# Kernel optimization log

Hardware: AMD Instinct MI355X
Metric: run time of the kernel (lower is better)

The kernel has to match this reference:

```python
import jax, jax.numpy as jnp
import numpy as np

K, S, B, D = 6, 257, 64, 1024   # blocks, seq, batch, d_model
H, DR = 16, 256                  # heads, pruned dim (d_model/reduction)
HD = DR // H                     # head_dim = 16
T = 0.1
EPS = 1e-5


def _ln(x, w, b):
    mu = jnp.mean(x, axis=-1, keepdims=True)
    var = jnp.var(x, axis=-1, keepdims=True)
    return (x - mu) * jax.lax.rsqrt(var + EPS) * w + b


def _quick_gelu(x):
    return x * jax.nn.sigmoid(1.702 * x)


def _block(x, ipw, ipb, opw, opb, l1w, l1b, l2w, l2b, fw, fb, cw, cb):
    # x: (S, B, D)
    h = _ln(x, l1w, l1b)
    qkv = jnp.einsum('sbe,fe->sbf', h, ipw) + ipb          # (S, B, 3*DR)
    q, k, v = jnp.split(qkv, 3, axis=-1)                    # each (S, B, DR)
    # (S, B*H, HD) -> (B*H, S, HD); row-major reshape matches torch .view
    q = q.reshape(S, B * H, HD).swapaxes(0, 1) / jnp.sqrt(jnp.asarray(HD, x.dtype))
    k = k.reshape(S, B * H, HD).swapaxes(0, 1)
    v = v.reshape(S, B * H, HD).swapaxes(0, 1)
    attn = jax.nn.softmax(jnp.einsum('bte,bse->bts', q, k), axis=-1)  # (B*H, S, S)
    o = jnp.einsum('bts,bse->bte', attn, v)                 # (B*H, S, HD)
    o = o.swapaxes(0, 1).reshape(S, B, DR)
    o = jnp.einsum('sbe,fe->sbf', o, opw) + opb             # (S, B, D)
    x = x + o
    h2 = _ln(x, l2w, l2b)
    m = _quick_gelu(jnp.einsum('sbe,fe->sbf', h2, fw) + fb)
    m = jnp.einsum('sbe,fe->sbf', m, cw) + cb
    return x + m


def setup_inputs() -> dict:
    key = jax.random.key(0)
    ks = jax.random.split(key, 10)
    p = 0.02
    return {
        'hook_inputs': jax.random.normal(ks[0], (K, S, B, D), jnp.float32),
        'alpha': jax.random.normal(ks[1], (K,), jnp.float32),
        'in_proj_w': jax.random.normal(ks[2], (K, 3 * DR, D), jnp.float32) * p,
        'in_proj_b': jnp.zeros((K, 3 * DR), jnp.float32),
        'out_proj_w': jax.random.normal(ks[3], (K, D, DR), jnp.float32) * p,
        'out_proj_b': jnp.zeros((K, D), jnp.float32),
        'ln1_w': jnp.ones((K, D), jnp.float32),
        'ln1_b': jnp.zeros((K, D), jnp.float32),
        'ln2_w': jnp.ones((K, D), jnp.float32),
        'ln2_b': jnp.zeros((K, D), jnp.float32),
        'fc_w': jax.random.normal(ks[4], (K, D, D), jnp.float32) * p,
        'fc_b': jnp.zeros((K, D), jnp.float32),
        'cproj_w': jax.random.normal(ks[5], (K, D, D), jnp.float32) * p,
        'cproj_b': jnp.zeros((K, D), jnp.float32),
        'ln_post_w': jnp.ones((D,), jnp.float32),
        'ln_post_b': jnp.zeros((D,), jnp.float32),
        'proj': jax.random.normal(ks[6], (D, 768), jnp.float32) * p,
    }


def reference(hook_inputs, alpha, in_proj_w, in_proj_b, out_proj_w, out_proj_b,
              ln1_w, ln1_b, ln2_w, ln2_b, fc_w, fc_b, cproj_w, cproj_b,
              ln_post_w, ln_post_b, proj):
    Wm = jax.nn.sigmoid(alpha / T)
    x = None
    for i in range(K):  # small fixed number of structurally distinct blocks
        res = hook_inputs[i]
        if i == 0:
            x = res
        else:
            x = Wm[i] * res + (1.0 - Wm[i]) * x
        x = _block(x, in_proj_w[i], in_proj_b[i], out_proj_w[i], out_proj_b[i],
                   ln1_w[i], ln1_b[i], ln2_w[i], ln2_b[i],
                   fc_w[i], fc_b[i], cproj_w[i], cproj_b[i])
    x = x.transpose(1, 0, 2)                 # (B, S, D)
    x = _ln(x, ln_post_w, ln_post_b)
    x = jnp.einsum('bsd,dp->bsp', x, proj)   # (B, S, 768)
    return x
```

## Files before the change

kernel.cpp:

```cpp
#include <hip/hip_runtime.h>
#include <hip/hip_bf16.h>
#include <cstdint>
#include <cstddef>

#define KBLK 6
#define SL 257
#define BA 64
#define DM 1024
#define NHEAD 16
#define DRED 256
#define HDM 16
#define MR (SL * BA)
#define MP 16512
#define LNEPS 1e-5f

typedef __hip_bfloat16 bf16;
typedef __attribute__((ext_vector_type(8))) short short8;
typedef __attribute__((ext_vector_type(4))) short short4_t;
typedef __attribute__((ext_vector_type(4))) float f32x4;

__device__ __forceinline__ void gld_lds16(const void* g, void* l) {
  __builtin_amdgcn_global_load_lds(
      (const __attribute__((address_space(1))) unsigned int*)g,
      (__attribute__((address_space(3))) unsigned int*)l, 16, 0, 0);
}

__device__ __forceinline__ float bf2f(short s) {
  bf16 t = *reinterpret_cast<bf16*>(&s);
  return __bfloat162float(t);
}
__device__ __forceinline__ short f2bf(float f) {
  bf16 t = __float2bfloat16(f);
  return *reinterpret_cast<short*>(&t);
}

__global__ __launch_bounds__(256) void cast_all_kernel(
    const float* __restrict__ ipw, const float* __restrict__ opw,
    const float* __restrict__ fcw, const float* __restrict__ cpw,
    const float* __restrict__ proj,
    bf16* __restrict__ wq, bf16* __restrict__ wo, bf16* __restrict__ wfc,
    bf16* __restrict__ wcp, bf16* __restrict__ wpj) {
  const int blk = blockIdx.x;
  const int tid = threadIdx.x;
  const float* src;
  bf16* dst;
  int base;
  bool tr = false;
  if (blk < 2304)      { src = ipw; dst = wq;  base = blk * 2048; }
  else if (blk < 3072) { src = opw; dst = wo;  base = (blk - 2304) * 2048; }
  else if (blk < 6144) { src = fcw; dst = wfc; base = (blk - 3072) * 2048; }
  else if (blk < 9216) { src = cpw; dst = wcp; base = (blk - 6144) * 2048; }
  else                 { src = proj; dst = wpj; base = (blk - 9216) * 2048; tr = true; }
  const int idx = base + tid * 8;
  short8 o;
  if (!tr) {
    float4 a = *(const float4*)(src + idx);
    float4 b = *(const float4*)(src + idx + 4);
    o[0] = f2bf(a.x); o[1] = f2bf(a.y); o[2] = f2bf(a.z); o[3] = f2bf(a.w);
    o[4] = f2bf(b.x); o[5] = f2bf(b.y); o[6] = f2bf(b.z); o[7] = f2bf(b.w);
  } else {
    int n = idx >> 10, k = idx & 1023;
#pragma unroll
    for (int e = 0; e < 8; ++e) o[e] = f2bf(src[(size_t)(k + e) * 768 + n]);
  }
  *(short8*)(dst + idx) = o;
}

template <int MODE>
__global__ __launch_bounds__(256) void ln_kernel(
    const float* __restrict__ hook,
    bf16* __restrict__ x, bf16* __restrict__ hout,
    const float* __restrict__ w, const float* __restrict__ bb) {
  const int row = blockIdx.x;
  const int tid = threadIdx.x;
  const size_t base = (size_t)row * DM + tid * 4;
  float vals[4];
  if (MODE == 0) {
    float4 v = *(const float4*)(hook + base);
    vals[0] = v.x; vals[1] = v.y; vals[2] = v.z; vals[3] = v.w;
    short4_t pk;
#pragma unroll
    for (int j = 0; j < 4; ++j) pk[j] = f2bf(vals[j]);
    *(short4_t*)&x[base] = pk;
  } else {
    short4_t xv = *(const short4_t*)&x[base];
#pragma unroll
    for (int j = 0; j < 4; ++j) vals[j] = bf2f(xv[j]);
  }
  float s1 = vals[0] + vals[1] + vals[2] + vals[3];
  float s2 = vals[0] * vals[0] + vals[1] * vals[1] + vals[2] * vals[2] + vals[3] * vals[3];
#pragma unroll
  for (int o = 32; o >= 1; o >>= 1) {
    s1 += __shfl_down(s1, o);
    s2 += __shfl_down(s2, o);
  }
  __shared__ float red[8];
  if ((tid & 63) == 0) {
    red[tid >> 6] = s1;
    red[4 + (tid >> 6)] = s2;
  }
  __syncthreads();
  s1 = red[0] + red[1] + red[2] + red[3];
  s2 = red[4] + red[5] + red[6] + red[7];
  const float mu = s1 * (1.f / DM);
  const float rs = rsqrtf(s2 * (1.f / DM) - mu * mu + LNEPS);
  size_t orow = row;
  if (MODE == 3) {
    int s = row >> 6, b2 = row & 63;
    orow = (size_t)b2 * SL + s;
  }
  const int c = tid * 4;
  short4_t pk;
#pragma unroll
  for (int j = 0; j < 4; ++j)
    pk[j] = f2bf((vals[j] - mu) * rs * w[c + j] + bb[c + j]);
  *(short4_t*)((char*)hout + (orow * DM + c) * 2) = pk;
}

__global__ __launch_bounds__(256) void attn_mfma_kernel(const bf16* __restrict__ qkv,
                                                        bf16* __restrict__ obuf) {
  __shared__ __align__(16) short ql[272][24];
  __shared__ __align__(16) short kl[272][24];
  __shared__ __align__(16) short vt[16][296];
  __shared__ __align__(16) short pl[4][16][40];
  const int bh = blockIdx.x;
  const int b = bh >> 4, h = bh & 15;
  const int tid = threadIdx.x;
  const int wave = tid >> 6, lane = tid & 63;
  const int g = lane >> 4, qi = lane & 15;

  const short8 zero8 = {0, 0, 0, 0, 0, 0, 0, 0};
  const f32x4 fzero = {0.f, 0.f, 0.f, 0.f};

  for (int task = tid; task < 1632; task += 256) {
    int a, rem;
    if (task < 544) { a = 0; rem = task; }
    else if (task < 1088) { a = 1; rem = task - 544; }
    else { a = 2; rem = task - 1088; }
    int row = rem >> 1, half = rem & 1;
    short8 v = zero8;
    if (row < SL)
      v = *(const short8*)((const short*)qkv + (size_t)(row * BA + b) * 768 + a * 256 + h * 16 + half * 8);
    if (a == 0) *(short8*)&ql[row][half * 8] = v;
    else if (a == 1) *(short8*)&kl[row][half * 8] = v;
    else {
#pragma unroll
      for (int j = 0; j < 8; ++j) vt[half * 8 + j][row] = v[j];
    }
  }
  for (int i = tid; i < 16 * 24; i += 256) vt[i / 24][272 + (i % 24)] = 0;
  __syncthreads();

  for (int t = wave; t < 17; t += 4) {
    short8 bq = zero8;
    if (g < 2) bq = *(const short8*)&ql[t * 16 + qi][g * 8];

    f32x4 st[18];
#pragma unroll
    for (int t2 = 0; t2 < 17; ++t2) {
      short8 ak = zero8;
      if (g < 2) ak = *(const short8*)&kl[t2 * 16 + qi][g * 8];
      st[t2] = __builtin_amdgcn_mfma_f32_16x16x32_bf16(ak, bq, fzero, 0, 0, 0);
    }
    float mx = -1e30f;
#pragma unroll
    for (int t2 = 0; t2 < 17; ++t2) {
#pragma unroll
      for (int r = 0; r < 4; ++r) {
        int s = t2 * 16 + g * 4 + r;
        float v = (s <= 256) ? st[t2][r] * 0.25f : -1e30f;
        st[t2][r] = v;
        mx = fmaxf(mx, v);
      }
    }
    mx = fmaxf(mx, __shfl_xor(mx, 16));
    mx = fmaxf(mx, __shfl_xor(mx, 32));
    float ls = 0.f;
#pragma unroll
    for (int t2 = 0; t2 < 17; ++t2) {
#pragma unroll
      for (int r = 0; r < 4; ++r) {
        float p = __expf(st[t2][r] - mx);
        st[t2][r] = p;
        ls += p;
      }
    }
    ls += __shfl_xor(ls, 16);
    ls += __shfl_xor(ls, 32);
    const float inv = 1.f / ls;
#pragma unroll
    for (int t2 = 0; t2 < 17; ++t2)
#pragma unroll
      for (int r = 0; r < 4; ++r) st[t2][r] *= inv;
    st[17] = fzero;

    f32x4 acc = fzero;
#pragma unroll
    for (int tt = 0; tt < 9; ++tt) {
#pragma unroll
      for (int hh = 0; hh < 2; ++hh) {
        int t2 = tt * 2 + hh;
        short4_t pk;
#pragma unroll
        for (int r = 0; r < 4; ++r) pk[r] = f2bf(st[t2][r]);
        *(short4_t*)&pl[wave][qi][hh * 16 + g * 4] = pk;
      }
      short8 pa = *(const short8*)&pl[wave][qi][g * 8];
      short8 bv = *(const short8*)&vt[qi][tt * 32 + g * 8];
      acc = __builtin_amdgcn_mfma_f32_16x16x32_bf16(pa, bv, acc, 0, 0, 0);
    }
#pragma unroll
    for (int r = 0; r < 4; ++r) {
      int qr = t * 16 + g * 4 + r;
      if (qr < SL)
        obuf[(size_t)(qr * BA + b) * DRED + h * 16 + qi] = __float2bfloat16(acc[r]);
    }
  }
}

template <int EPI>
__global__ __launch_bounds__(256, 4) void gemm_kernel(
    const bf16* __restrict__ A, int lda,
    const bf16* __restrict__ Bw, int ldb,
    const float* __restrict__ bias,
    void* __restrict__ C, int ldc,
    int Kdim, int Mreal,
    const float* __restrict__ hook, const float* __restrict__ alphap, int kidx) {
  __shared__ char lds[32768];
  const int tid = threadIdx.x;
  const int wave = tid >> 6, lane = tid & 63;
  const int lrow = lane & 15, lk = lane >> 4;
  const int wr = wave >> 1, wc = wave & 1;

  const int gx = gridDim.x, gy = gridDim.y;
  const int nwg = gx * gy;
  const int orig = blockIdx.y * gx + blockIdx.x;
  const int q = nwg >> 3, r = nwg & 7;
  const int xcd = orig & 7, idx = orig >> 3;
  const int wgid = (xcd < r ? xcd * (q + 1) : r * (q + 1) + (xcd - r) * q) + idx;
  const int m0 = (wgid / gy) * 128;
  const int n0 = (wgid % gy) * 128;

  f32x4 acc[4][4];
  const f32x4 zero = {0.f, 0.f, 0.f, 0.f};
#pragma unroll
  for (int i = 0; i < 4; ++i)
#pragma unroll
    for (int j = 0; j < 4; ++j) acc[i][j] = zero;

  const int nk = Kdim >> 6;

  for (int kt = 0; kt < nk; ++kt) {
    const int k0 = kt << 6;
#pragma unroll
    for (int j = 0; j < 4; ++j) {
      int c = wave * 256 + j * 64 + lane;
      int row = c >> 3, segp = c & 7;
      int seg = segp ^ (row & 7);
      const bf16* ga = A + (size_t)(m0 + row) * lda + k0 + seg * 8;
      gld_lds16(ga, &lds[(wave * 256 + j * 64) * 16]);
      const bf16* gb = Bw + (size_t)(n0 + row) * ldb + k0 + seg * 8;
      gld_lds16(gb, &lds[16384 + (wave * 256 + j * 64) * 16]);
    }
    __syncthreads();
    const char* aL = &lds[0];
    const char* bL = aL + 16384;
#pragma unroll
    for (int kh = 0; kh < 2; ++kh) {
      short8 af[4], bfr[4];
#pragma unroll
      for (int i = 0; i < 4; ++i) {
        int rr = wr * 64 + i * 16 + lrow;
        int seg = kh * 4 + lk;
        af[i] = *(const short8*)(aL + rr * 128 + ((seg ^ (rr & 7)) << 4));
      }
#pragma unroll
      for (int j = 0; j < 4; ++j) {
        int rr = wc * 64 + j * 16 + lrow;
        int seg = kh * 4 + lk;
        bfr[j] = *(const short8*)(bL + rr * 128 + ((seg ^ (rr & 7)) << 4));
      }
#pragma unroll
      for (int i = 0; i < 4; ++i)
#pragma unroll
        for (int j = 0; j < 4; ++j)
          acc[i][j] = __builtin_amdgcn_mfma_f32_16x16x32_bf16(bfr[j], af[i], acc[i][j], 0, 0, 0);
    }
    __syncthreads();
  }

  float wmg = 0.f, omg = 0.f;
  if (EPI == 4) {
    wmg = 1.f / (1.f + __expf(-alphap[kidx] * 10.f));
    omg = 1.f - wmg;
  }
#pragma unroll
  for (int i = 0; i < 4; ++i) {
    const int row = m0 + wr * 64 + i * 16 + lrow;
    if (row >= Mreal) continue;
#pragma unroll
    for (int j = 0; j < 4; ++j) {
      const int col = n0 + wc * 64 + j * 16 + lk * 4;
      const size_t off = (size_t)row * ldc + col;
      float bv[4] = {0.f, 0.f, 0.f, 0.f};
      if (bias) {
        float4 b4 = *(const float4*)&bias[col];
        bv[0] = b4.x; bv[1] = b4.y; bv[2] = b4.z; bv[3] = b4.w;
      }
      float v[4];
#pragma unroll
      for (int rr = 0; rr < 4; ++rr) v[rr] = acc[i][j][rr] + bv[rr];
      if (EPI == 0) {
        float4 o4 = {v[0], v[1], v[2], v[3]};
        *(float4*)((float*)C + off) = o4;
      } else if (EPI == 2) {
        short4_t pk;
#pragma unroll
        for (int rr = 0; rr < 4; ++rr)
          pk[rr] = f2bf(v[rr] / (1.f + __expf(-1.702f * v[rr])));
        *(short4_t*)((bf16*)C + off) = pk;
      } else if (EPI == 3) {
        short4_t pk;
#pragma unroll
        for (int rr = 0; rr < 4; ++rr) pk[rr] = f2bf(v[rr]);
        *(short4_t*)((bf16*)C + off) = pk;
      } else if (EPI == 1) {
        short4_t xv = *(const short4_t*)((const bf16*)C + off);
        short4_t pk;
#pragma unroll
        for (int rr = 0; rr < 4; ++rr) pk[rr] = f2bf(bf2f(xv[rr]) + v[rr]);
        *(short4_t*)((bf16*)C + off) = pk;
      } else {
        short4_t xv = *(const short4_t*)((const bf16*)C + off);
        float4 h4 = *(const float4*)&hook[off];
        float hk[4] = {h4.x, h4.y, h4.z, h4.w};
        short4_t pk;
#pragma unroll
        for (int rr = 0; rr < 4; ++rr)
          pk[rr] = f2bf(wmg * hk[rr] + omg * (bf2f(xv[rr]) + v[rr]));
        *(short4_t*)((bf16*)C + off) = pk;
      }
    }
  }
}

extern "C" void kernel_launch(void* const* d_in, const int* in_sizes, int n_in,
                              void* d_out, int out_size, void* d_ws, size_t ws_size,
                              hipStream_t stream) {
  const float* hook = (const float*)d_in[0];
  const float* alpha = (const float*)d_in[1];
  const float* ipw = (const float*)d_in[2];
  const float* ipb = (const float*)d_in[3];
  const float* opw = (const float*)d_in[4];
  const float* opb = (const float*)d_in[5];
  const float* l1w = (const float*)d_in[6];
  const float* l1b = (const float*)d_in[7];
  const float* l2w = (const float*)d_in[8];
  const float* l2b = (const float*)d_in[9];
  const float* fcw = (const float*)d_in[10];
  const float* fcb = (const float*)d_in[11];
  const float* cpw = (const float*)d_in[12];
  const float* cpb = (const float*)d_in[13];
  const float* lpw = (const float*)d_in[14];
  const float* lpb = (const float*)d_in[15];
  const float* proj = (const float*)d_in[16];

  char* ws = (char*)d_ws;
  size_t off = 0;
  bf16* x = (bf16*)(ws + off); off += (size_t)MP * DM * 2;
  bf16* hbuf = (bf16*)(ws + off); off += (size_t)MP * DM * 2;
  bf16* qkv = (bf16*)(ws + off);
  bf16* mbuf = (bf16*)qkv;
  off += (size_t)MP * 1024 * 2;
  bf16* obuf = (bf16*)(ws + off); off += (size_t)MP * DRED * 2;
  bf16* wq = (bf16*)(ws + off); off += (size_t)KBLK * 768 * DM * 2;
  bf16* wo = (bf16*)(ws + off); off += (size_t)KBLK * DM * DRED * 2;
  bf16* wfc = (bf16*)(ws + off); off += (size_t)KBLK * DM * DM * 2;
  bf16* wcp = (bf16*)(ws + off); off += (size_t)KBLK * DM * DM * 2;
  bf16* wpj = (bf16*)(ws + off); off += (size_t)768 * DM * 2;

  cast_all_kernel<<<9600, 256, 0, stream>>>(ipw, opw, fcw, cpw, proj,
                                            wq, wo, wfc, wcp, wpj);

  const dim3 gq(MP / 128, 768 / 128);
  const dim3 gm(MP / 128, DM / 128);

  for (int i = 0; i < KBLK; ++i) {
    if (i == 0)
      ln_kernel<0><<<MR, 256, 0, stream>>>(hook, x, hbuf, l1w, l1b);
    else
      ln_kernel<2><<<MR, 256, 0, stream>>>(nullptr, x, hbuf, l1w + i * DM, l1b + i * DM);
    gemm_kernel<3><<<gq, 256, 0, stream>>>(hbuf, DM, wq + (size_t)i * 768 * DM, DM,
                                           ipb + i * 768, qkv, 768, DM, MR,
                                           nullptr, nullptr, 0);
    attn_mfma_kernel<<<BA * NHEAD, 256, 0, stream>>>(qkv, obuf);
    gemm_kernel<1><<<gm, 256, 0, stream>>>(obuf, DRED, wo + (size_t)i * DM * DRED, DRED,
                                           opb + i * DM, x, DM, DRED, MR,
                                           nullptr, nullptr, 0);
    ln_kernel<2><<<MR, 256, 0, stream>>>(nullptr, x, hbuf, l2w + i * DM, l2b + i * DM);
    gemm_kernel<2><<<gm, 256, 0, stream>>>(hbuf, DM, wfc + (size_t)i * DM * DM, DM,
                                           fcb + i * DM, mbuf, DM, DM, MR,
                                           nullptr, nullptr, 0);
    if (i + 1 < KBLK)
      gemm_kernel<4><<<gm, 256, 0, stream>>>(mbuf, DM, wcp + (size_t)i * DM * DM, DM,
                                             cpb + i * DM, x, DM, DM, MR,
                                             hook + (size_t)(i + 1) * MR * DM, alpha, i + 1);
    else
      gemm_kernel<1><<<gm, 256, 0, stream>>>(mbuf, DM, wcp + (size_t)i * DM * DM, DM,
                                             cpb + i * DM, x, DM, DM, MR,
                                             nullptr, nullptr, 0);
  }
  ln_kernel<3><<<MR, 256, 0, stream>>>(nullptr, x, hbuf, lpw, lpb);
  gemm_kernel<0><<<gq, 256, 0, stream>>>(hbuf, DM, wpj, DM, nullptr,
                                         (float*)d_out, 768, DM, MR,
                                         nullptr, nullptr, 0);
}
```

Measured before the change: 1.797 ms.

## Fuse all per-block kernels into one persistent cooperative megakernel with grid syncs

```diff
diff --git a/kernel.cpp b/kernel.cpp
--- a/kernel.cpp
+++ b/kernel.cpp
@@ -1,7 +1,10 @@
 #include <hip/hip_runtime.h>
 #include <hip/hip_bf16.h>
+#include <hip/hip_cooperative_groups.h>
 #include <cstdint>
 #include <cstddef>
+
+namespace cg = cooperative_groups;
 
 #define KBLK 6
 #define SL 257
@@ -66,282 +69,326 @@
   *(short8*)(dst + idx) = o;
 }
 
-template <int MODE>
-__global__ __launch_bounds__(256) void ln_kernel(
-    const float* __restrict__ hook,
-    bf16* __restrict__ x, bf16* __restrict__ hout,
-    const float* __restrict__ w, const float* __restrict__ bb) {
-  const int row = blockIdx.x;
+union __align__(16) MegaLds {
+  char gemm[32768];
+  struct {
+    short kl[272][24];
+    short vt[16][296];
+    short pl[4][16][40];
+  } at;
+  float red[8];
+};
+
+__device__ __forceinline__ void ph_ln(int mode, int nwg, int wg,
+    const float* __restrict__ hk, bf16* __restrict__ x, bf16* __restrict__ hout,
+    const float* __restrict__ w, const float* __restrict__ bb, float* red) {
   const int tid = threadIdx.x;
-  const size_t base = (size_t)row * DM + tid * 4;
-  float vals[4];
-  if (MODE == 0) {
-    float4 v = *(const float4*)(hook + base);
-    vals[0] = v.x; vals[1] = v.y; vals[2] = v.z; vals[3] = v.w;
+  for (int row = wg; row < MR; row += nwg) {
+    const size_t base = (size_t)row * DM + tid * 4;
+    float vals[4];
+    if (mode == 0) {
+      float4 v = *(const float4*)(hk + base);
+      vals[0] = v.x; vals[1] = v.y; vals[2] = v.z; vals[3] = v.w;
+      short4_t pk;
+#pragma unroll
+      for (int j = 0; j < 4; ++j) pk[j] = f2bf(vals[j]);
+      *(short4_t*)&x[base] = pk;
+    } else {
+      short4_t xv = *(const short4_t*)&x[base];
+#pragma unroll
+      for (int j = 0; j < 4; ++j) vals[j] = bf2f(xv[j]);
+    }
+    float s1 = vals[0] + vals[1] + vals[2] + vals[3];
+    float s2 = vals[0] * vals[0] + vals[1] * vals[1] + vals[2] * vals[2] + vals[3] * vals[3];
+#pragma unroll
+    for (int o = 32; o >= 1; o >>= 1) {
+      s1 += __shfl_down(s1, o);
+      s2 += __shfl_down(s2, o);
+    }
+    if ((tid & 63) == 0) {
+      red[tid >> 6] = s1;
+      red[4 + (tid >> 6)] = s2;
+    }
+    __syncthreads();
+    s1 = red[0] + red[1] + red[2] + red[3];
+    s2 = red[4] + red[5] + red[6] + red[7];
+    const float mu = s1 * (1.f / DM);
+    const float rs = rsqrtf(s2 * (1.f / DM) - mu * mu + LNEPS);
+    size_t orow = row;
+    if (mode == 3) {
+      int s = row >> 6, b2 = row & 63;
+      orow = (size_t)b2 * SL + s;
+    }
+    const int c = tid * 4;
     short4_t pk;
 #pragma unroll
-    for (int j = 0; j < 4; ++j) pk[j] = f2bf(vals[j]);
-    *(short4_t*)&x[base] = pk;
-  } else {
-    short4_t xv = *(const short4_t*)&x[base];
-#pragma unroll
-    for (int j = 0; j < 4; ++j) vals[j] = bf2f(xv[j]);
-  }
-  float s1 = vals[0] + vals[1] + vals[2] + vals[3];
-  float s2 = vals[0] * vals[0] + vals[1] * vals[1] + vals[2] * vals[2] + vals[3] * vals[3];
-#pragma unroll
-  for (int o = 32; o >= 1; o >>= 1) {
-    s1 += __shfl_down(s1, o);
-    s2 += __shfl_down(s2, o);
-  }
-  __shared__ float red[8];
-  if ((tid & 63) == 0) {
-    red[tid >> 6] = s1;
-    red[4 + (tid >> 6)] = s2;
-  }
-  __syncthreads();
-  s1 = red[0] + red[1] + red[2] + red[3];
-  s2 = red[4] + red[5] + red[6] + red[7];
-  const float mu = s1 * (1.f / DM);
-  const float rs = rsqrtf(s2 * (1.f / DM) - mu * mu + LNEPS);
-  size_t orow = row;
-  if (MODE == 3) {
-    int s = row >> 6, b2 = row & 63;
-    orow = (size_t)b2 * SL + s;
-  }
-  const int c = tid * 4;
-  short4_t pk;
-#pragma unroll
-  for (int j = 0; j < 4; ++j)
-    pk[j] = f2bf((vals[j] - mu) * rs * w[c + j] + bb[c + j]);
-  *(short4_t*)((char*)hout + (orow * DM + c) * 2) = pk;
-}
-
-__global__ __launch_bounds__(256) void attn_mfma_kernel(const bf16* __restrict__ qkv,
-                                                        bf16* __restrict__ obuf) {
-  __shared__ __align__(16) short ql[272][24];
-  __shared__ __align__(16) short kl[272][24];
-  __shared__ __align__(16) short vt[16][296];
-  __shared__ __align__(16) short pl[4][16][40];
-  const int bh = blockIdx.x;
-  const int b = bh >> 4, h = bh & 15;
+    for (int j = 0; j < 4; ++j)
+      pk[j] = f2bf((vals[j] - mu) * rs * w[c + j] + bb[c + j]);
+    *(short4_t*)((char*)hout + (orow * DM + c) * 2) = pk;
+    __syncthreads();
+  }
+}
+
+__device__ __forceinline__ void ph_attn(int nwg, int wg, MegaLds* L,
+                                        const bf16* __restrict__ qkv,
+                                        bf16* __restrict__ obuf) {
   const int tid = threadIdx.x;
   const int wave = tid >> 6, lane = tid & 63;
   const int g = lane >> 4, qi = lane & 15;
-
   const short8 zero8 = {0, 0, 0, 0, 0, 0, 0, 0};
   const f32x4 fzero = {0.f, 0.f, 0.f, 0.f};
 
-  for (int task = tid; task < 1632; task += 256) {
-    int a, rem;
-    if (task < 544) { a = 0; rem = task; }
-    else if (task < 1088) { a = 1; rem = task - 544; }
-    else { a = 2; rem = task - 1088; }
-    int row = rem >> 1, half = rem & 1;
-    short8 v = zero8;
-    if (row < SL)
-      v = *(const short8*)((const short*)qkv + (size_t)(row * BA + b) * 768 + a * 256 + h * 16 + half * 8);
-    if (a == 0) *(short8*)&ql[row][half * 8] = v;
-    else if (a == 1) *(short8*)&kl[row][half * 8] = v;
-    else {
-#pragma unroll
-      for (int j = 0; j < 8; ++j) vt[half * 8 + j][row] = v[j];
-    }
-  }
-  for (int i = tid; i < 16 * 24; i += 256) vt[i / 24][272 + (i % 24)] = 0;
-  __syncthreads();
-
-  for (int t = wave; t < 17; t += 4) {
-    short8 bq = zero8;
-    if (g < 2) bq = *(const short8*)&ql[t * 16 + qi][g * 8];
-
-    f32x4 st[18];
-#pragma unroll
-    for (int t2 = 0; t2 < 17; ++t2) {
-      short8 ak = zero8;
-      if (g < 2) ak = *(const short8*)&kl[t2 * 16 + qi][g * 8];
-      st[t2] = __builtin_amdgcn_mfma_f32_16x16x32_bf16(ak, bq, fzero, 0, 0, 0);
-    }
-    float mx = -1e30f;
-#pragma unroll
-    for (int t2 = 0; t2 < 17; ++t2) {
+  for (int bh = wg; bh < BA * NHEAD; bh += nwg) {
+    const int b = bh >> 4, h = bh & 15;
+    for (int task = tid; task < 1088; task += 256) {
+      int a = (task < 544) ? 1 : 2;
+      int rem = (task < 544) ? task : task - 544;
+      int row = rem >> 1, half = rem & 1;
+      short8 v = zero8;
+      if (row < SL)
+        v = *(const short8*)((const short*)qkv + (size_t)(row * BA + b) * 768 + a * 256 + h * 16 + half * 8);
+      if (a == 1) *(short8*)&L->at.kl[row][half * 8] = v;
+      else {
+#pragma unroll
+        for (int j = 0; j < 8; ++j) L->at.vt[half * 8 + j][row] = v[j];
+      }
+    }
+    for (int i = tid; i < 16 * 24; i += 256) L->at.vt[i / 24][272 + (i % 24)] = 0;
+    __syncthreads();
+
+    for (int t = wave; t < 17; t += 4) {
+      const int qrow = t * 16 + qi;
+      short8 bq = zero8;
+      if (g < 2 && qrow < SL)
+        bq = *(const short8*)((const short*)qkv + (size_t)(qrow * BA + b) * 768 + h * 16 + g * 8);
+
+      f32x4 st[18];
+#pragma unroll
+      for (int t2 = 0; t2 < 17; ++t2) {
+        short8 ak = zero8;
+        if (g < 2) ak = *(const short8*)&L->at.kl[t2 * 16 + qi][g * 8];
+        st[t2] = __builtin_amdgcn_mfma_f32_16x16x32_bf16(ak, bq, fzero, 0, 0, 0);
+      }
+      float mx = -1e30f;
+#pragma unroll
+      for (int t2 = 0; t2 < 17; ++t2) {
+#pragma unroll
+        for (int r = 0; r < 4; ++r) {
+          int s = t2 * 16 + g * 4 + r;
+          float v = (s <= 256) ? st[t2][r] * 0.25f : -1e30f;
+          st[t2][r] = v;
+          mx = fmaxf(mx, v);
+        }
+      }
+      mx = fmaxf(mx, __shfl_xor(mx, 16));
+      mx = fmaxf(mx, __shfl_xor(mx, 32));
+      float ls = 0.f;
+#pragma unroll
+      for (int t2 = 0; t2 < 17; ++t2) {
+#pragma unroll
+        for (int r = 0; r < 4; ++r) {
+          float p = __expf(st[t2][r] - mx);
+          st[t2][r] = p;
+          ls += p;
+        }
+      }
+      ls += __shfl_xor(ls, 16);
+      ls += __shfl_xor(ls, 32);
+      const float inv = 1.f / ls;
+#pragma unroll
+      for (int t2 = 0; t2 < 17; ++t2)
+#pragma unroll
+        for (int r = 0; r < 4; ++r) st[t2][r] *= inv;
+      st[17] = fzero;
+
+      f32x4 acc = fzero;
+#pragma unroll
+      for (int tt = 0; tt < 9; ++tt) {
+#pragma unroll
+        for (int hh = 0; hh < 2; ++hh) {
+          int t2 = tt * 2 + hh;
+          short4_t pk;
+#pragma unroll
+          for (int r = 0; r < 4; ++r) pk[r] = f2bf(st[t2][r]);
+          *(short4_t*)&L->at.pl[wave][qi][hh * 16 + g * 4] = pk;
+        }
+        short8 pa = *(const short8*)&L->at.pl[wave][qi][g * 8];
+        short8 bv = *(const short8*)&L->at.vt[qi][tt * 32 + g * 8];
+        acc = __builtin_amdgcn_mfma_f32_16x16x32_bf16(pa, bv, acc, 0, 0, 0);
+      }
 #pragma unroll
       for (int r = 0; r < 4; ++r) {
-        int s = t2 * 16 + g * 4 + r;
-        float v = (s <= 256) ? st[t2][r] * 0.25f : -1e30f;
-        st[t2][r] = v;
-        mx = fmaxf(mx, v);
-      }
-    }
-    mx = fmaxf(mx, __shfl_xor(mx, 16));
-    mx = fmaxf(mx, __shfl_xor(mx, 32));
-    float ls = 0.f;
-#pragma unroll
-    for (int t2 = 0; t2 < 17; ++t2) {
-#pragma unroll
-      for (int r = 0; r < 4; ++r) {
-        float p = __expf(st[t2][r] - mx);
-        st[t2][r] = p;
-        ls += p;
-      }
-    }
-    ls += __shfl_xor(ls, 16);
-    ls += __shfl_xor(ls, 32);
-    const float inv = 1.f / ls;
-#pragma unroll
-    for (int t2 = 0; t2 < 17; ++t2)
-#pragma unroll
-      for (int r = 0; r < 4; ++r) st[t2][r] *= inv;
-    st[17] = fzero;
-
-    f32x4 acc = fzero;
-#pragma unroll
-    for (int tt = 0; tt < 9; ++tt) {
-#pragma unroll
-      for (int hh = 0; hh < 2; ++hh) {
-        int t2 = tt * 2 + hh;
-        short4_t pk;
-#pragma unroll
-        for (int r = 0; r < 4; ++r) pk[r] = f2bf(st[t2][r]);
-        *(short4_t*)&pl[wave][qi][hh * 16 + g * 4] = pk;
-      }
-      short8 pa = *(const short8*)&pl[wave][qi][g * 8];
-      short8 bv = *(const short8*)&vt[qi][tt * 32 + g * 8];
-      acc = __builtin_amdgcn_mfma_f32_16x16x32_bf16(pa, bv, acc, 0, 0, 0);
-    }
-#pragma unroll
-    for (int r = 0; r < 4; ++r) {
-      int qr = t * 16 + g * 4 + r;
-      if (qr < SL)
-        obuf[(size_t)(qr * BA + b) * DRED + h * 16 + qi] = __float2bfloat16(acc[r]);
-    }
+        int qr = t * 16 + g * 4 + r;
+        if (qr < SL)
+          obuf[(size_t)(qr * BA + b) * DRED + h * 16 + qi] = __float2bfloat16(acc[r]);
+      }
+    }
+    __syncthreads();
   }
 }
 
 template <int EPI>
-__global__ __launch_bounds__(256, 4) void gemm_kernel(
+__device__ __forceinline__ void ph_gemm(int nwg, int wg, char* lds,
     const bf16* __restrict__ A, int lda,
     const bf16* __restrict__ Bw, int ldb,
     const float* __restrict__ bias,
     void* __restrict__ C, int ldc,
-    int Kdim, int Mreal,
+    int Kdim, int nT, int ntiles,
     const float* __restrict__ hook, const float* __restrict__ alphap, int kidx) {
-  __shared__ char lds[32768];
   const int tid = threadIdx.x;
   const int wave = tid >> 6, lane = tid & 63;
   const int lrow = lane & 15, lk = lane >> 4;
   const int wr = wave >> 1, wc = wave & 1;
-
-  const int gx = gridDim.x, gy = gridDim.y;
-  const int nwg = gx * gy;
-  const int orig = blockIdx.y * gx + blockIdx.x;
-  const int q = nwg >> 3, r = nwg & 7;
-  const int xcd = orig & 7, idx = orig >> 3;
-  const int wgid = (xcd < r ? xcd * (q + 1) : r * (q + 1) + (xcd - r) * q) + idx;
-  const int m0 = (wgid / gy) * 128;
-  const int n0 = (wgid % gy) * 128;
-
-  f32x4 acc[4][4];
-  const f32x4 zero = {0.f, 0.f, 0.f, 0.f};
-#pragma unroll
-  for (int i = 0; i < 4; ++i)
-#pragma unroll
-    for (int j = 0; j < 4; ++j) acc[i][j] = zero;
-
+  const int q = ntiles >> 3, r = ntiles & 7;
   const int nk = Kdim >> 6;
-
-  for (int kt = 0; kt < nk; ++kt) {
-    const int k0 = kt << 6;
-#pragma unroll
-    for (int j = 0; j < 4; ++j) {
-      int c = wave * 256 + j * 64 + lane;
-      int row = c >> 3, segp = c & 7;
-      int seg = segp ^ (row & 7);
-      const bf16* ga = A + (size_t)(m0 + row) * lda + k0 + seg * 8;
-      gld_lds16(ga, &lds[(wave * 256 + j * 64) * 16]);
-      const bf16* gb = Bw + (size_t)(n0 + row) * ldb + k0 + seg * 8;
-      gld_lds16(gb, &lds[16384 + (wave * 256 + j * 64) * 16]);
-    }
-    __syncthreads();
-    const char* aL = &lds[0];
-    const char* bL = aL + 16384;
-#pragma unroll
-    for (int kh = 0; kh < 2; ++kh) {
-      short8 af[4], bfr[4];
-#pragma unroll
-      for (int i = 0; i < 4; ++i) {
-        int rr = wr * 64 + i * 16 + lrow;
-        int seg = kh * 4 + lk;
-        af[i] = *(const short8*)(aL + rr * 128 + ((seg ^ (rr & 7)) << 4));
-      }
-#pragma unroll
-      for (int j = 0; j < 4; ++j) {
-        int rr = wc * 64 + j * 16 + lrow;
-        int seg = kh * 4 + lk;
-        bfr[j] = *(const short8*)(bL + rr * 128 + ((seg ^ (rr & 7)) << 4));
-      }
-#pragma unroll
-      for (int i = 0; i < 4; ++i)
-#pragma unroll
-        for (int j = 0; j < 4; ++j)
-          acc[i][j] = __builtin_amdgcn_mfma_f32_16x16x32_bf16(bfr[j], af[i], acc[i][j], 0, 0, 0);
-    }
-    __syncthreads();
-  }
 
   float wmg = 0.f, omg = 0.f;
   if (EPI == 4) {
     wmg = 1.f / (1.f + __expf(-alphap[kidx] * 10.f));
     omg = 1.f - wmg;
   }
-#pragma unroll
-  for (int i = 0; i < 4; ++i) {
-    const int row = m0 + wr * 64 + i * 16 + lrow;
-    if (row >= Mreal) continue;
-#pragma unroll
-    for (int j = 0; j < 4; ++j) {
-      const int col = n0 + wc * 64 + j * 16 + lk * 4;
-      const size_t off = (size_t)row * ldc + col;
-      float bv[4] = {0.f, 0.f, 0.f, 0.f};
-      if (bias) {
-        float4 b4 = *(const float4*)&bias[col];
-        bv[0] = b4.x; bv[1] = b4.y; bv[2] = b4.z; bv[3] = b4.w;
-      }
-      float v[4];
-#pragma unroll
-      for (int rr = 0; rr < 4; ++rr) v[rr] = acc[i][j][rr] + bv[rr];
-      if (EPI == 0) {
-        float4 o4 = {v[0], v[1], v[2], v[3]};
-        *(float4*)((float*)C + off) = o4;
-      } else if (EPI == 2) {
-        short4_t pk;
-#pragma unroll
-        for (int rr = 0; rr < 4; ++rr)
-          pk[rr] = f2bf(v[rr] / (1.f + __expf(-1.702f * v[rr])));
-        *(short4_t*)((bf16*)C + off) = pk;
-      } else if (EPI == 3) {
-        short4_t pk;
-#pragma unroll
-        for (int rr = 0; rr < 4; ++rr) pk[rr] = f2bf(v[rr]);
-        *(short4_t*)((bf16*)C + off) = pk;
-      } else if (EPI == 1) {
-        short4_t xv = *(const short4_t*)((const bf16*)C + off);
-        short4_t pk;
-#pragma unroll
-        for (int rr = 0; rr < 4; ++rr) pk[rr] = f2bf(bf2f(xv[rr]) + v[rr]);
-        *(short4_t*)((bf16*)C + off) = pk;
-      } else {
-        short4_t xv = *(const short4_t*)((const bf16*)C + off);
-        float4 h4 = *(const float4*)&hook[off];
-        float hk[4] = {h4.x, h4.y, h4.z, h4.w};
-        short4_t pk;
-#pragma unroll
-        for (int rr = 0; rr < 4; ++rr)
-          pk[rr] = f2bf(wmg * hk[rr] + omg * (bf2f(xv[rr]) + v[rr]));
-        *(short4_t*)((bf16*)C + off) = pk;
-      }
-    }
-  }
+
+  for (int t0 = wg; t0 < ntiles; t0 += nwg) {
+    const int xcd = t0 & 7, idx = t0 >> 3;
+    const int wgid = (xcd < r ? xcd * (q + 1) : r * (q + 1) + (xcd - r) * q) + idx;
+    const int m0 = (wgid / nT) * 128;
+    const int n0 = (wgid % nT) * 128;
+
+    f32x4 acc[4][4];
+    const f32x4 zero = {0.f, 0.f, 0.f, 0.f};
+#pragma unroll
+    for (int i = 0; i < 4; ++i)
+#pragma unroll
+      for (int j = 0; j < 4; ++j) acc[i][j] = zero;
+
+    for (int kt = 0; kt < nk; ++kt) {
+      const int k0 = kt << 6;
+#pragma unroll
+      for (int j = 0; j < 4; ++j) {
+        int c = wave * 256 + j * 64 + lane;
+        int row = c >> 3, segp = c & 7;
+        int seg = segp ^ (row & 7);
+        gld_lds16(A + (size_t)(m0 + row) * lda + k0 + seg * 8, &lds[c * 16]);
+        gld_lds16(Bw + (size_t)(n0 + row) * ldb + k0 + seg * 8, &lds[16384 + c * 16]);
+      }
+      __syncthreads();
+#pragma unroll
+      for (int kh = 0; kh < 2; ++kh) {
+        short8 af[4], bfr[4];
+#pragma unroll
+        for (int i = 0; i < 4; ++i) {
+          int rr = wr * 64 + i * 16 + lrow;
+          int seg = kh * 4 + lk;
+          af[i] = *(const short8*)(lds + rr * 128 + ((seg ^ (rr & 7)) << 4));
+        }
+#pragma unroll
+        for (int j = 0; j < 4; ++j) {
+          int rr = wc * 64 + j * 16 + lrow;
+          int seg = kh * 4 + lk;
+          bfr[j] = *(const short8*)(lds + 16384 + rr * 128 + ((seg ^ (rr & 7)) << 4));
+        }
+#pragma unroll
+        for (int i = 0; i < 4; ++i)
+#pragma unroll
+          for (int j = 0; j < 4; ++j)
+            acc[i][j] = __builtin_amdgcn_mfma_f32_16x16x32_bf16(bfr[j], af[i], acc[i][j], 0, 0, 0);
+      }
+      __syncthreads();
+    }
+
+#pragma unroll
+    for (int i = 0; i < 4; ++i) {
+      const int row = m0 + wr * 64 + i * 16 + lrow;
+      if (row >= MR) continue;
+#pragma unroll
+      for (int j = 0; j < 4; ++j) {
+        const int col = n0 + wc * 64 + j * 16 + lk * 4;
+        const size_t off = (size_t)row * ldc + col;
+        float bv[4] = {0.f, 0.f, 0.f, 0.f};
+        if (bias) {
+          float4 b4 = *(const float4*)&bias[col];
+          bv[0] = b4.x; bv[1] = b4.y; bv[2] = b4.z; bv[3] = b4.w;
+        }
+        float v[4];
+#pragma unroll
+        for (int rr = 0; rr < 4; ++rr) v[rr] = acc[i][j][rr] + bv[rr];
+        if (EPI == 0) {
+          float4 o4 = {v[0], v[1], v[2], v[3]};
+          *(float4*)((float*)C + off) = o4;
+        } else if (EPI == 2) {
+          short4_t pk;
+#pragma unroll
+          for (int rr = 0; rr < 4; ++rr)
+            pk[rr] = f2bf(v[rr] / (1.f + __expf(-1.702f * v[rr])));
+          *(short4_t*)((bf16*)C + off) = pk;
+        } else if (EPI == 3) {
+          short4_t pk;
+#pragma unroll
+          for (int rr = 0; rr < 4; ++rr) pk[rr] = f2bf(v[rr]);
+          *(short4_t*)((bf16*)C + off) = pk;
+        } else if (EPI == 1) {
+          short4_t xv = *(const short4_t*)((const bf16*)C + off);
+          short4_t pk;
+#pragma unroll
+          for (int rr = 0; rr < 4; ++rr) pk[rr] = f2bf(bf2f(xv[rr]) + v[rr]);
+          *(short4_t*)((bf16*)C + off) = pk;
+        } else {
+          short4_t xv = *(const short4_t*)((const bf16*)C + off);
+          float4 h4 = *(const float4*)&hook[off];
+          float hk[4] = {h4.x, h4.y, h4.z, h4.w};
+          short4_t pk;
+#pragma unroll
+          for (int rr = 0; rr < 4; ++rr)
+            pk[rr] = f2bf(wmg * hk[rr] + omg * (bf2f(xv[rr]) + v[rr]));
+          *(short4_t*)((bf16*)C + off) = pk;
+        }
+      }
+    }
+  }
+}
+
+__global__ __launch_bounds__(256, 4) void mega_kernel(
+    const float* hook, const float* alpha,
+    const float* ipb, const float* opb,
+    const float* l1w, const float* l1b, const float* l2w, const float* l2b,
+    const float* fcb, const float* cpb, const float* lpw, const float* lpb,
+    bf16* x, bf16* hbuf, bf16* qkv, bf16* obuf,
+    const bf16* wq, const bf16* wo, const bf16* wfc, const bf16* wcp, const bf16* wpj,
+    float* outp) {
+  cg::grid_group grid = cg::this_grid();
+  __shared__ MegaLds L;
+  const int wg = blockIdx.x, nwg = gridDim.x;
+  bf16* mbuf = qkv;
+
+  for (int i = 0; i < KBLK; ++i) {
+    ph_ln(i == 0 ? 0 : 2, nwg, wg, hook, x, hbuf, l1w + i * DM, l1b + i * DM, L.red);
+    grid.sync();
+    ph_gemm<3>(nwg, wg, L.gemm, hbuf, DM, wq + (size_t)i * 768 * DM, DM,
+               ipb + i * 768, qkv, 768, DM, 6, 774, nullptr, nullptr, 0);
+    grid.sync();
+    ph_attn(nwg, wg, &L, qkv, obuf);
+    grid.sync();
+    ph_gemm<1>(nwg, wg, L.gemm, obuf, DRED, wo + (size_t)i * DM * DRED, DRED,
+               opb + i * DM, x, DM, DRED, 8, 1032, nullptr, nullptr, 0);
+    grid.sync();
+    ph_ln(2, nwg, wg, nullptr, x, hbuf, l2w + i * DM, l2b + i * DM, L.red);
+    grid.sync();
+    ph_gemm<2>(nwg, wg, L.gemm, hbuf, DM, wfc + (size_t)i * DM * DM, DM,
+               fcb + i * DM, mbuf, DM, DM, 8, 1032, nullptr, nullptr, 0);
+    grid.sync();
+    if (i + 1 < KBLK)
+      ph_gemm<4>(nwg, wg, L.gemm, mbuf, DM, wcp + (size_t)i * DM * DM, DM,
+                 cpb + i * DM, x, DM, DM, 8, 1032,
+                 hook + (size_t)(i + 1) * MR * DM, alpha, i + 1);
+    else
+      ph_gemm<1>(nwg, wg, L.gemm, mbuf, DM, wcp + (size_t)i * DM * DM, DM,
+                 cpb + i * DM, x, DM, DM, 8, 1032, nullptr, nullptr, 0);
+    grid.sync();
+  }
+  ph_ln(3, nwg, wg, nullptr, x, hbuf, lpw, lpb, L.red);
+  grid.sync();
+  ph_gemm<0>(nwg, wg, L.gemm, hbuf, DM, wpj, DM, nullptr,
+             outp, 768, DM, 6, 774, nullptr, nullptr, 0);
 }
 
 extern "C" void kernel_launch(void* const* d_in, const int* in_sizes, int n_in,
@@ -369,9 +416,7 @@
   size_t off = 0;
   bf16* x = (bf16*)(ws + off); off += (size_t)MP * DM * 2;
   bf16* hbuf = (bf16*)(ws + off); off += (size_t)MP * DM * 2;
-  bf16* qkv = (bf16*)(ws + off);
-  bf16* mbuf = (bf16*)qkv;
-  off += (size_t)MP * 1024 * 2;
+  bf16* qkv = (bf16*)(ws + off); off += (size_t)MP * 1024 * 2;
   bf16* obuf = (bf16*)(ws + off); off += (size_t)MP * DRED * 2;
   bf16* wq = (bf16*)(ws + off); off += (size_t)KBLK * 768 * DM * 2;
   bf16* wo = (bf16*)(ws + off); off += (size_t)KBLK * DM * DRED * 2;
@@ -382,36 +427,20 @@
   cast_all_kernel<<<9600, 256, 0, stream>>>(ipw, opw, fcw, cpw, proj,
                                             wq, wo, wfc, wcp, wpj);
 
-  const dim3 gq(MP / 128, 768 / 128);
-  const dim3 gm(MP / 128, DM / 128);
-
-  for (int i = 0; i < KBLK; ++i) {
-    if (i == 0)
-      ln_kernel<0><<<MR, 256, 0, stream>>>(hook, x, hbuf, l1w, l1b);
-    else
-      ln_kernel<2><<<MR, 256, 0, stream>>>(nullptr, x, hbuf, l1w + i * DM, l1b + i * DM);
-    gemm_kernel<3><<<gq, 256, 0, stream>>>(hbuf, DM, wq + (size_t)i * 768 * DM, DM,
-                                           ipb + i * 768, qkv, 768, DM, MR,
-                                           nullptr, nullptr, 0);
-    attn_mfma_kernel<<<BA * NHEAD, 256, 0, stream>>>(qkv, obuf);
-    gemm_kernel<1><<<gm, 256, 0, stream>>>(obuf, DRED, wo + (size_t)i * DM * DRED, DRED,
-                                           opb + i * DM, x, DM, DRED, MR,
-                                           nullptr, nullptr, 0);
-    ln_kernel<2><<<MR, 256, 0, stream>>>(nullptr, x, hbuf, l2w + i * DM, l2b + i * DM);
-    gemm_kernel<2><<<gm, 256, 0, stream>>>(hbuf, DM, wfc + (size_t)i * DM * DM, DM,
-                                           fcb + i * DM, mbuf, DM, DM, MR,
-                                           nullptr, nullptr, 0);
-    if (i + 1 < KBLK)
-      gemm_kernel<4><<<gm, 256, 0, stream>>>(mbuf, DM, wcp + (size_t)i * DM * DM, DM,
-                                             cpb + i * DM, x, DM, DM, MR,
-                                             hook + (size_t)(i + 1) * MR * DM, alpha, i + 1);
-    else
-      gemm_kernel<1><<<gm, 256, 0, stream>>>(mbuf, DM, wcp + (size_t)i * DM * DM, DM,
-                                             cpb + i * DM, x, DM, DM, MR,
-                                             nullptr, nullptr, 0);
-  }
-  ln_kernel<3><<<MR, 256, 0, stream>>>(nullptr, x, hbuf, lpw, lpb);
-  gemm_kernel<0><<<gq, 256, 0, stream>>>(hbuf, DM, wpj, DM, nullptr,
-                                         (float*)d_out, 768, DM, MR,
-                                         nullptr, nullptr, 0);
-}
+  int occ = 0;
+  hipOccupancyMaxActiveBlocksPerMultiprocessor(&occ, mega_kernel, 256, 0);
+  int gw = occ * 256;
+  if (gw > 1024) gw = 1024;
+  if (gw < 256) gw = 256;
+  float* outp = (float*)d_out;
+
+  void* params[] = {
+      (void*)&hook, (void*)&alpha, (void*)&ipb, (void*)&opb,
+      (void*)&l1w, (void*)&l1b, (void*)&l2w, (void*)&l2b,
+      (void*)&fcb, (void*)&cpb, (void*)&lpw, (void*)&lpb,
+      (void*)&x, (void*)&hbuf, (void*)&qkv, (void*)&obuf,
+      (void*)&wq, (void*)&wo, (void*)&wfc, (void*)&wcp, (void*)&wpj,
+      (void*)&outp};
+  hipLaunchCooperativeKernel((void*)mega_kernel, dim3(gw), dim3(256),
+                             params, 0, stream);
+}
```

Result: slower. 5.144 ms (+186.3%).

## Fuse LayerNorm into residual GEMM epilogues via last-block-per-panel counters

Applied to the files above, without the earlier changes.

```diff
diff --git a/kernel.cpp b/kernel.cpp
--- a/kernel.cpp
+++ b/kernel.cpp
@@ -13,6 +13,8 @@
 #define MR (SL * BA)
 #define MP 16512
 #define LNEPS 1e-5f
+#define NPANEL 129
+#define NCNT (12 * NPANEL)
 
 typedef __hip_bfloat16 bf16;
 typedef __attribute__((ext_vector_type(8))) short short8;
@@ -39,9 +41,12 @@
     const float* __restrict__ fcw, const float* __restrict__ cpw,
     const float* __restrict__ proj,
     bf16* __restrict__ wq, bf16* __restrict__ wo, bf16* __restrict__ wfc,
-    bf16* __restrict__ wcp, bf16* __restrict__ wpj) {
+    bf16* __restrict__ wcp, bf16* __restrict__ wpj, int* __restrict__ cnt) {
   const int blk = blockIdx.x;
   const int tid = threadIdx.x;
+  if (blk == 0) {
+    for (int z = tid; z < NCNT; z += 256) cnt[z] = 0;
+  }
   const float* src;
   bf16* dst;
   int base;
@@ -66,8 +71,7 @@
   *(short8*)(dst + idx) = o;
 }
 
-template <int MODE>
-__global__ __launch_bounds__(256) void ln_kernel(
+__global__ __launch_bounds__(256) void ln0_kernel(
     const float* __restrict__ hook,
     bf16* __restrict__ x, bf16* __restrict__ hout,
     const float* __restrict__ w, const float* __restrict__ bb) {
@@ -75,18 +79,12 @@
   const int tid = threadIdx.x;
   const size_t base = (size_t)row * DM + tid * 4;
   float vals[4];
-  if (MODE == 0) {
-    float4 v = *(const float4*)(hook + base);
-    vals[0] = v.x; vals[1] = v.y; vals[2] = v.z; vals[3] = v.w;
-    short4_t pk;
-#pragma unroll
-    for (int j = 0; j < 4; ++j) pk[j] = f2bf(vals[j]);
-    *(short4_t*)&x[base] = pk;
-  } else {
-    short4_t xv = *(const short4_t*)&x[base];
-#pragma unroll
-    for (int j = 0; j < 4; ++j) vals[j] = bf2f(xv[j]);
-  }
+  float4 v = *(const float4*)(hook + base);
+  vals[0] = v.x; vals[1] = v.y; vals[2] = v.z; vals[3] = v.w;
+  short4_t pk0;
+#pragma unroll
+  for (int j = 0; j < 4; ++j) pk0[j] = f2bf(vals[j]);
+  *(short4_t*)&x[base] = pk0;
   float s1 = vals[0] + vals[1] + vals[2] + vals[3];
   float s2 = vals[0] * vals[0] + vals[1] * vals[1] + vals[2] * vals[2] + vals[3] * vals[3];
 #pragma unroll
@@ -104,17 +102,12 @@
   s2 = red[4] + red[5] + red[6] + red[7];
   const float mu = s1 * (1.f / DM);
   const float rs = rsqrtf(s2 * (1.f / DM) - mu * mu + LNEPS);
-  size_t orow = row;
-  if (MODE == 3) {
-    int s = row >> 6, b2 = row & 63;
-    orow = (size_t)b2 * SL + s;
-  }
   const int c = tid * 4;
   short4_t pk;
 #pragma unroll
   for (int j = 0; j < 4; ++j)
     pk[j] = f2bf((vals[j] - mu) * rs * w[c + j] + bb[c + j]);
-  *(short4_t*)((char*)hout + (orow * DM + c) * 2) = pk;
+  *(short4_t*)((char*)hout + ((size_t)row * DM + c) * 2) = pk;
 }
 
 __global__ __launch_bounds__(256) void attn_mfma_kernel(const bf16* __restrict__ qkv,
@@ -218,14 +211,16 @@
   }
 }
 
-template <int EPI>
+template <int EPI, int FLN>
 __global__ __launch_bounds__(256, 4) void gemm_kernel(
     const bf16* __restrict__ A, int lda,
     const bf16* __restrict__ Bw, int ldb,
     const float* __restrict__ bias,
     void* __restrict__ C, int ldc,
     int Kdim, int Mreal,
-    const float* __restrict__ hook, const float* __restrict__ alphap, int kidx) {
+    const float* __restrict__ hook, const float* __restrict__ alphap, int kidx,
+    const float* __restrict__ lnw, const float* __restrict__ lnb,
+    bf16* __restrict__ lnout, int* __restrict__ cnt) {
   __shared__ char lds[32768];
   const int tid = threadIdx.x;
   const int wave = tid >> 6, lane = tid & 63;
@@ -257,14 +252,10 @@
       int c = wave * 256 + j * 64 + lane;
       int row = c >> 3, segp = c & 7;
       int seg = segp ^ (row & 7);
-      const bf16* ga = A + (size_t)(m0 + row) * lda + k0 + seg * 8;
-      gld_lds16(ga, &lds[(wave * 256 + j * 64) * 16]);
-      const bf16* gb = Bw + (size_t)(n0 + row) * ldb + k0 + seg * 8;
-      gld_lds16(gb, &lds[16384 + (wave * 256 + j * 64) * 16]);
+      gld_lds16(A + (size_t)(m0 + row) * lda + k0 + seg * 8, &lds[c * 16]);
+      gld_lds16(Bw + (size_t)(n0 + row) * ldb + k0 + seg * 8, &lds[16384 + c * 16]);
     }
     __syncthreads();
-    const char* aL = &lds[0];
-    const char* bL = aL + 16384;
 #pragma unroll
     for (int kh = 0; kh < 2; ++kh) {
       short8 af[4], bfr[4];
@@ -272,13 +263,13 @@
       for (int i = 0; i < 4; ++i) {
         int rr = wr * 64 + i * 16 + lrow;
         int seg = kh * 4 + lk;
-        af[i] = *(const short8*)(aL + rr * 128 + ((seg ^ (rr & 7)) << 4));
+        af[i] = *(const short8*)(lds + rr * 128 + ((seg ^ (rr & 7)) << 4));
       }
 #pragma unroll
       for (int j = 0; j < 4; ++j) {
         int rr = wc * 64 + j * 16 + lrow;
         int seg = kh * 4 + lk;
-        bfr[j] = *(const short8*)(bL + rr * 128 + ((seg ^ (rr & 7)) << 4));
+        bfr[j] = *(const short8*)(lds + 16384 + rr * 128 + ((seg ^ (rr & 7)) << 4));
       }
 #pragma unroll
       for (int i = 0; i < 4; ++i)
@@ -339,6 +330,59 @@
         for (int rr = 0; rr < 4; ++rr)
           pk[rr] = f2bf(wmg * hk[rr] + omg * (bf2f(xv[rr]) + v[rr]));
         *(short4_t*)((bf16*)C + off) = pk;
+      }
+    }
+  }
+
+  if (FLN != 0) {
+    __shared__ int lastf;
+    __threadfence();
+    if (tid == 0)
+      lastf = (atomicAdd(&cnt[m0 >> 7], 1) == (int)gy - 1) ? 1 : 0;
+    __syncthreads();
+    if (lastf) {
+      __threadfence();
+      const bf16* xr = (const bf16*)C;
+      for (int r2 = wave; r2 < 128; r2 += 4) {
+        const int row = m0 + r2;
+        if (row >= MR) break;
+        const short8* xp = (const short8*)(xr + (size_t)row * ldc);
+        short8 v0 = xp[lane * 2];
+        short8 v1 = xp[lane * 2 + 1];
+        float f[16];
+        float s1 = 0.f, s2 = 0.f;
+#pragma unroll
+        for (int e = 0; e < 8; ++e) {
+          f[e] = bf2f(v0[e]);
+          f[8 + e] = bf2f(v1[e]);
+        }
+#pragma unroll
+        for (int e = 0; e < 16; ++e) {
+          s1 += f[e];
+          s2 += f[e] * f[e];
+        }
+#pragma unroll
+        for (int o = 32; o >= 1; o >>= 1) {
+          s1 += __shfl_down(s1, o);
+          s2 += __shfl_down(s2, o);
+        }
+        s1 = __shfl(s1, 0);
+        s2 = __shfl(s2, 0);
+        const float mu = s1 * (1.f / DM);
+        const float rs = rsqrtf(s2 * (1.f / DM) - mu * mu + LNEPS);
+        const int c0 = lane * 16;
+        short8 o0, o1;
+#pragma unroll
+        for (int e = 0; e < 16; ++e) {
+          float t = (f[e] - mu) * rs * lnw[c0 + e] + lnb[c0 + e];
+          if (e < 8) o0[e] = f2bf(t);
+          else o1[e - 8] = f2bf(t);
+        }
+        size_t orow = row;
+        if (FLN == 2) orow = (size_t)(row & 63) * SL + (row >> 6);
+        short8* op = (short8*)(lnout + orow * DM + c0);
+        op[0] = o0;
+        op[1] = o1;
       }
     }
   }
@@ -378,40 +422,46 @@
   bf16* wfc = (bf16*)(ws + off); off += (size_t)KBLK * DM * DM * 2;
   bf16* wcp = (bf16*)(ws + off); off += (size_t)KBLK * DM * DM * 2;
   bf16* wpj = (bf16*)(ws + off); off += (size_t)768 * DM * 2;
+  int* cnt = (int*)(ws + off); off += NCNT * 4;
 
   cast_all_kernel<<<9600, 256, 0, stream>>>(ipw, opw, fcw, cpw, proj,
-                                            wq, wo, wfc, wcp, wpj);
+                                            wq, wo, wfc, wcp, wpj, cnt);
 
   const dim3 gq(MP / 128, 768 / 128);
   const dim3 gm(MP / 128, DM / 128);
 
   for (int i = 0; i < KBLK; ++i) {
     if (i == 0)
-      ln_kernel<0><<<MR, 256, 0, stream>>>(hook, x, hbuf, l1w, l1b);
+      ln0_kernel<<<MR, 256, 0, stream>>>(hook, x, hbuf, l1w, l1b);
+    gemm_kernel<3, 0><<<gq, 256, 0, stream>>>(hbuf, DM, wq + (size_t)i * 768 * DM, DM,
+                                              ipb + i * 768, qkv, 768, DM, MR,
+                                              nullptr, nullptr, 0,
+                                              nullptr, nullptr, nullptr, nullptr);
+    attn_mfma_kernel<<<BA * NHEAD, 256, 0, stream>>>(qkv, obuf);
+    gemm_kernel<1, 1><<<gm, 256, 0, stream>>>(obuf, DRED, wo + (size_t)i * DM * DRED, DRED,
+                                              opb + i * DM, x, DM, DRED, MR,
+                                              nullptr, nullptr, 0,
+                                              l2w + i * DM, l2b + i * DM, hbuf,
+                                              cnt + (2 * i) * NPANEL);
+    gemm_kernel<2, 0><<<gm, 256, 0, stream>>>(hbuf, DM, wfc + (size_t)i * DM * DM, DM,
+                                              fcb + i * DM, mbuf, DM, DM, MR,
+                                              nullptr, nullptr, 0,
+                                              nullptr, nullptr, nullptr, nullptr);
+    if (i + 1 < KBLK)
+      gemm_kernel<4, 1><<<gm, 256, 0, stream>>>(mbuf, DM, wcp + (size_t)i * DM * DM, DM,
+                                                cpb + i * DM, x, DM, DM, MR,
+                                                hook + (size_t)(i + 1) * MR * DM, alpha, i + 1,
+                                                l1w + (i + 1) * DM, l1b + (i + 1) * DM, hbuf,
+                                                cnt + (2 * i + 1) * NPANEL);
     else
-      ln_kernel<2><<<MR, 256, 0, stream>>>(nullptr, x, hbuf, l1w + i * DM, l1b + i * DM);
-    gemm_kernel<3><<<gq, 256, 0, stream>>>(hbuf, DM, wq + (size_t)i * 768 * DM, DM,
-                                           ipb + i * 768, qkv, 768, DM, MR,
-                                           nullptr, nullptr, 0);
-    attn_mfma_kernel<<<BA * NHEAD, 256, 0, stream>>>(qkv, obuf);
-    gemm_kernel<1><<<gm, 256, 0, stream>>>(obuf, DRED, wo + (size_t)i * DM * DRED, DRED,
-                                           opb + i * DM, x, DM, DRED, MR,
-                                           nullptr, nullptr, 0);
-    ln_kernel<2><<<MR, 256, 0, stream>>>(nullptr, x, hbuf, l2w + i * DM, l2b + i * DM);
-    gemm_kernel<2><<<gm, 256, 0, stream>>>(hbuf, DM, wfc + (size_t)i * DM * DM, DM,
-                                           fcb + i * DM, mbuf, DM, DM, MR,
-                                           nullptr, nullptr, 0);
-    if (i + 1 < KBLK)
-      gemm_kernel<4><<<gm, 256, 0, stream>>>(mbuf, DM, wcp + (size_t)i * DM * DM, DM,
-                                             cpb + i * DM, x, DM, DM, MR,
-                                             hook + (size_t)(i + 1) * MR * DM, alpha, i + 1);
-    else
-      gemm_kernel<1><<<gm, 256, 0, stream>>>(mbuf, DM, wcp + (size_t)i * DM * DM, DM,
-                                             cpb + i * DM, x, DM, DM, MR,
-                                             nullptr, nullptr, 0);
-  }
-  ln_kernel<3><<<MR, 256, 0, stream>>>(nullptr, x, hbuf, lpw, lpb);
-  gemm_kernel<0><<<gq, 256, 0, stream>>>(hbuf, DM, wpj, DM, nullptr,
-                                         (float*)d_out, 768, DM, MR,
-                                         nullptr, nullptr, 0);
-}
+      gemm_kernel<1, 2><<<gm, 256, 0, stream>>>(mbuf, DM, wcp + (size_t)i * DM * DM, DM,
+                                                cpb + i * DM, x, DM, DM, MR,
+                                                nullptr, nullptr, 0,
+                                                lpw, lpb, hbuf,
+                                                cnt + (2 * i + 1) * NPANEL);
+  }
+  gemm_kernel<0, 0><<<gq, 256, 0, stream>>>(hbuf, DM, wpj, DM, nullptr,
+                                            (float*)d_out, 768, DM, MR,
+                                            nullptr, nullptr, 0,
+                                            nullptr, nullptr, nullptr, nullptr);
+}
```

New measurement: 4.427 ms. +146.4%, slower.
